# Kernel optimization log

Hardware: AMD Instinct MI355X
Metric: run time of the kernel (lower is better)

## Reference

```python
import jax, jax.numpy as jnp
import numpy as np


def setup_inputs() -> dict:
    key = jax.random.key(0)
    k1, k2, k3 = jax.random.split(key, 3)
    B, N, D = 4, 4096, 1024
    x = jax.random.normal(k1, (B, N, D), dtype=jnp.float32)
    # torch nn.Linear default init ~ U(-1/sqrt(D), 1/sqrt(D)); scale normals similarly
    scale = 1.0 / np.sqrt(D)
    Wq = jax.random.normal(k2, (D, D), dtype=jnp.float32) * scale
    Wk = jax.random.normal(k3, (D, D), dtype=jnp.float32) * scale
    return {"x": x, "Wq": Wq, "Wk": Wk}


def reference(x, Wq, Wk):
    # torch Linear: y = x @ W.T (weight shape [out, in])
    D = x.shape[-1]
    q = jnp.einsum('bnd,ed->bne', x, Wq)  # [B,N,D]
    k = jnp.einsum('bnd,ed->bne', x, Wk)  # [B,N,D]
    scores = jnp.einsum('bqd,bkd->bqk', q, k) / jnp.sqrt(jnp.float32(D))
    attn = jax.nn.softmax(scores, axis=-1)  # [B,N,N]
    return jnp.einsum('bqk,bkd->bqd', attn, x)
```

## Files before the change

### kernel.cpp

```cpp
#include <hip/hip_runtime.h>
#include <stdint.h>
#include <math.h>

typedef __attribute__((ext_vector_type(8))) short short8;
typedef __attribute__((ext_vector_type(4))) float fx4;
typedef unsigned int u32;

#define MFMA16(a, b, c) __builtin_amdgcn_mfma_f32_16x16x32_bf16(a, b, c, 0, 0, 0)
#define SCL 0.04508422002777948f

#define CFENCE asm volatile("" ::: "memory")

__device__ __forceinline__ unsigned short f2bfu(float f) {
  unsigned u = __builtin_bit_cast(unsigned, f);
  u += 0x7fffu + ((u >> 16) & 1u);
  return (unsigned short)(u >> 16);
}

__device__ __forceinline__ float fast_exp2(float x) {
  float r;
  asm("v_exp_f32 %0, %1" : "=v"(r) : "v"(x));
  return r;
}

__device__ __forceinline__ void gl_lds16(const void* g, void* l) {
  __builtin_amdgcn_global_load_lds(
      (const __attribute__((address_space(1))) u32*)g,
      (__attribute__((address_space(3))) u32*)l, 16, 0, 0);
}

__device__ __forceinline__ void barx() {
  CFENCE;
  __builtin_amdgcn_s_barrier();
  CFENCE;
}

__global__ __launch_bounds__(256) void prep_kernel(const float* __restrict__ x,
                                                   unsigned short* __restrict__ xT,
                                                   unsigned short* __restrict__ xbf) {
  __shared__ float tile[64 * 65];
  const int b = blockIdx.z, n0 = blockIdx.x * 64, d0 = blockIdx.y * 64;
  const int tid = threadIdx.x;
  const float* xb = x + ((size_t)b * 4096 + n0) * 1024 + d0;
#pragma unroll
  for (int i = 0; i < 4; i++) {
    int idx = tid + 256 * i;
    int r = idx >> 4, c4 = (idx & 15) * 4;
    const float4 v = *(const float4*)(xb + (size_t)r * 1024 + c4);
    float* tp = &tile[r * 65 + c4];
    tp[0] = v.x; tp[1] = v.y; tp[2] = v.z; tp[3] = v.w;
    uint2 pkt;
    pkt.x = (u32)f2bfu(v.x) | ((u32)f2bfu(v.y) << 16);
    pkt.y = (u32)f2bfu(v.z) | ((u32)f2bfu(v.w) << 16);
    *(uint2*)(xbf + ((size_t)b * 4096 + n0 + r) * 1024 + d0 + c4) = pkt;
  }
  __syncthreads();
  unsigned short* xo = xT + ((size_t)b * 1024 + d0) * 4096 + n0;
#pragma unroll
  for (int i = 0; i < 4; i++) {
    int idx = tid + 256 * i;
    int dr = idx >> 4, n4 = (idx & 15) * 4;
    unsigned short h0 = f2bfu(tile[(n4 + 0) * 65 + dr]);
    unsigned short h1 = f2bfu(tile[(n4 + 1) * 65 + dr]);
    unsigned short h2 = f2bfu(tile[(n4 + 2) * 65 + dr]);
    unsigned short h3 = f2bfu(tile[(n4 + 3) * 65 + dr]);
    uint2 pkt;
    pkt.x = (u32)h0 | ((u32)h1 << 16);
    pkt.y = (u32)h2 | ((u32)h3 << 16);
    *(uint2*)(xo + (size_t)dr * 4096 + n4) = pkt;
  }
}

__global__ __launch_bounds__(256) void wconv_kernel(const float* __restrict__ Wq,
                                                    const float* __restrict__ Wk,
                                                    unsigned short* __restrict__ Wqb,
                                                    unsigned short* __restrict__ Wkb) {
  int gid = blockIdx.x * 256 + threadIdx.x;
  const float* s = (gid < 262144) ? Wq : Wk;
  unsigned short* d = (gid < 262144) ? Wqb : Wkb;
  int off = (gid & 262143) * 4;
  const float4 v = *(const float4*)(s + off);
  uint2 pkt;
  pkt.x = (u32)f2bfu(v.x) | ((u32)f2bfu(v.y) << 16);
  pkt.y = (u32)f2bfu(v.z) | ((u32)f2bfu(v.w) << 16);
  *(uint2*)(d + off) = pkt;
}


template <int ONES, int NT, int LDA, int LDB>
__device__ __forceinline__ void core128(const unsigned short* __restrict__ Ab,
                                        const unsigned short* __restrict__ Bb,
                                        short* lds, fx4 (&acc)[4][4], fx4 (&accl)[4]) {
  constexpr int BUFB = 49152;
  const int tid = threadIdx.x;
  const int wave = tid >> 6, lane = tid & 63;
  const int wm = wave >> 1, wn = wave & 1;
  const int quad = lane >> 4, l16 = lane & 15;
  char* lp = (char*)lds;

  const int sr0 = tid >> 3, so0 = (tid & 7) ^ (sr0 & 7);
  const int ga0 = sr0 * LDA + so0 * 8;
  const int ga1 = ga0 + 64 * LDA;
  const int gb0 = sr0 * LDB + so0 * 8;
  const int ld0 = tid * 16;

  const int cst0 = (quad ^ (l16 & 7)) * 16;
  const int cst1 = ((4 + quad) ^ (l16 & 7)) * 16;
  const int arb = (wm >> 1) * 16384 + (wm & 1) * 8192 + l16 * 128;
  const int brb = 32768 + wn * 8192 + l16 * 128;

  short8 ones;
#pragma unroll
  for (int i = 0; i < 8; i++) ones[i] = (short)0x3F80;
#pragma unroll
  for (int i = 0; i < 4; i++) {
    accl[i] = (fx4)0.f;
#pragma unroll
    for (int j = 0; j < 4; j++) acc[i][j] = (fx4)0.f;
  }

#define PV_STGA(halfb, rowadd, bufb, kte)                                          \
  do {                                                                             \
    gl_lds16(Ab + (size_t)(rowadd) * LDA + (kte) + ga0, lp + (bufb) + (halfb) + ld0); \
    gl_lds16(Ab + (size_t)(rowadd) * LDA + (kte) + ga1,                            \
             lp + (bufb) + (halfb) + ld0 + 8192);                                  \
  } while (0)
#define PV_STGB(halfb, rowadd, bufb, kte) \
  gl_lds16(Bb + (size_t)(rowadd) * LDB + (kte) + gb0, lp + (bufb) + 32768 + (halfb) + ld0)

  PV_STGB(0, 0, 0, 0);
  PV_STGA(0, 0, 0, 0);
  PV_STGA(16384, 128, 0, 0);
  PV_STGB(8192, 64, 0, 0);
  PV_STGB(0, 0, BUFB, 64);
  PV_STGA(0, 0, BUFB, 64);
  asm volatile("s_waitcnt vmcnt(3)" ::: "memory");
  barx();

  short8 af[4], bf0[4], bf1[4];
  for (int t = 0; t < NT; ++t) {
    const int cbo = (t & 1) * BUFB, nbo = cbo ^ BUFB;
    const int kt1 = ((t + 1) & (NT - 1)) * 64;
    const int kt2 = ((t + 2) & (NT - 1)) * 64;
#pragma unroll
    for (int mt = 0; mt < 2; mt++) {
      af[2 * mt] = *(const short8*)(lp + cbo + arb + mt * 2048 + cst0);
      af[2 * mt + 1] = *(const short8*)(lp + cbo + arb + mt * 2048 + cst1);
    }
#pragma unroll
    for (int nt = 0; nt < 2; nt++) {
      bf0[2 * nt] = *(const short8*)(lp + cbo + brb + nt * 2048 + cst0);
      bf0[2 * nt + 1] = *(const short8*)(lp + cbo + brb + nt * 2048 + cst1);
    }
    PV_STGA(16384, 128, nbo, kt1);
    barx();
    __builtin_amdgcn_s_setprio(1);
#pragma unroll
    for (int mt = 0; mt < 2; mt++) {
#pragma unroll
      for (int nt = 0; nt < 2; nt++) {
        acc[mt][nt] = MFMA16(af[2 * mt], bf0[2 * nt], acc[mt][nt]);
        acc[mt][nt] = MFMA16(af[2 * mt + 1], bf0[2 * nt + 1], acc[mt][nt]);
      }
      if (ONES) {
        accl[mt] = MFMA16(af[2 * mt], ones, accl[mt]);
        accl[mt] = MFMA16(af[2 * mt + 1], ones, accl[mt]);
      }
    }
    __builtin_amdgcn_s_setprio(0);
    barx();
#pragma unroll
    for (int nt = 0; nt < 2; nt++) {
      bf1[2 * nt] = *(const short8*)(lp + cbo + brb + (nt + 2) * 2048 + cst0);
      bf1[2 * nt + 1] = *(const short8*)(lp + cbo + brb + (nt + 2) * 2048 + cst1);
    }
    PV_STGB(8192, 64, nbo, kt1);
    barx();
    __builtin_amdgcn_s_setprio(1);
#pragma unroll
    for (int mt = 0; mt < 2; mt++)
#pragma unroll
      for (int nt = 0; nt < 2; nt++) {
        acc[mt][nt + 2] = MFMA16(af[2 * mt], bf1[2 * nt], acc[mt][nt + 2]);
        acc[mt][nt + 2] = MFMA16(af[2 * mt + 1], bf1[2 * nt + 1], acc[mt][nt + 2]);
      }
    __builtin_amdgcn_s_setprio(0);
    barx();
#pragma unroll
    for (int mt = 0; mt < 2; mt++) {
      af[2 * mt] = *(const short8*)(lp + cbo + arb + (mt + 2) * 2048 + cst0);
      af[2 * mt + 1] = *(const short8*)(lp + cbo + arb + (mt + 2) * 2048 + cst1);
    }
    PV_STGB(0, 0, cbo, kt2);
    barx();
    __builtin_amdgcn_s_setprio(1);
#pragma unroll
    for (int mt = 0; mt < 2; mt++) {
#pragma unroll
      for (int nt = 0; nt < 2; nt++) {
        acc[mt + 2][nt + 2] = MFMA16(af[2 * mt], bf1[2 * nt], acc[mt + 2][nt + 2]);
        acc[mt + 2][nt + 2] = MFMA16(af[2 * mt + 1], bf1[2 * nt + 1], acc[mt + 2][nt + 2]);
      }
      if (ONES) {
        accl[mt + 2] = MFMA16(af[2 * mt], ones, accl[mt + 2]);
        accl[mt + 2] = MFMA16(af[2 * mt + 1], ones, accl[mt + 2]);
      }
    }
    __builtin_amdgcn_s_setprio(0);
    barx();
    PV_STGA(0, 0, cbo, kt2);
    asm volatile("s_waitcnt vmcnt(3)" ::: "memory");
    barx();
    __builtin_amdgcn_s_setprio(1);
#pragma unroll
    for (int mt = 0; mt < 2; mt++)
#pragma unroll
      for (int nt = 0; nt < 2; nt++) {
        acc[mt + 2][nt] = MFMA16(af[2 * mt], bf0[2 * nt], acc[mt + 2][nt]);
        acc[mt + 2][nt] = MFMA16(af[2 * mt + 1], bf0[2 * nt + 1], acc[mt + 2][nt]);
      }
    __builtin_amdgcn_s_setprio(0);
    barx();
  }
#undef PV_STGA
#undef PV_STGB
}

__global__ __launch_bounds__(512) void proj_kernel(
    const unsigned short* __restrict__ xbf, const unsigned short* __restrict__ Wqb,
    const unsigned short* __restrict__ Wkb, unsigned short* __restrict__ Qo,
    unsigned short* __restrict__ Ko) {
  __shared__ __attribute__((aligned(16))) short lds[49152];
  const unsigned short* Wb = blockIdx.z ? Wkb : Wqb;
  unsigned short* O = blockIdx.z ? Ko : Qo;
  const int m0 = blockIdx.x * 256, e0 = blockIdx.y * 128;
  fx4 acc[4][4], accl[4];
  core128<0, 16, 1024, 1024>(xbf + (size_t)m0 * 1024, Wb + (size_t)e0 * 1024, lds, acc, accl);
  const int wave = threadIdx.x >> 6, lane = threadIdx.x & 63;
  const int wm = wave >> 1, wn = wave & 1;
  const int quad = lane >> 4, l16 = lane & 15;
#pragma unroll
  for (int mt = 0; mt < 4; mt++) {
    const int row = m0 + wm * 64 + mt * 16 + quad * 4;
#pragma unroll
    for (int nt = 0; nt < 4; nt++) {
      const int col = e0 + wn * 64 + nt * 16 + l16;
      unsigned short* op = O + (size_t)row * 1024 + col;
#pragma unroll
      for (int i = 0; i < 4; i++) op[(size_t)i * 1024] = f2bfu(acc[mt][nt][i]);
    }
  }
}

__global__ __launch_bounds__(512) void pv_kernel(
    const unsigned short* __restrict__ P, const unsigned short* __restrict__ xT,
    unsigned short* __restrict__ Ost, int bbase) {
  __shared__ __attribute__((aligned(16))) short lds[49152];
  const int bz = blockIdx.z, b = bbase + bz;
  const int m0 = blockIdx.x * 256, e0 = blockIdx.y * 128;
  const unsigned short* Ab = P + (size_t)bz * 4096 * 4096 + (size_t)m0 * 4096;
  const unsigned short* Bb = xT + (size_t)b * 1024 * 4096 + (size_t)e0 * 4096;
  fx4 acc[4][4], accl[4];
  core128<1, 64, 4096, 4096>(Ab, Bb, lds, acc, accl);
  unsigned short* O = Ost + (size_t)b * 4096 * 1024;
  const int wave = threadIdx.x >> 6, lane = threadIdx.x & 63;
  const int wm = wave >> 1, wn = wave & 1;
  const int quad = lane >> 4, l16 = lane & 15;
#pragma unroll
  for (int mt = 0; mt < 4; mt++) {
    const int row = m0 + wm * 64 + mt * 16 + quad * 4;
    const fx4 li = accl[mt];
    fx4 r;
#pragma unroll
    for (int i = 0; i < 4; i++) r[i] = __builtin_amdgcn_rcpf(li[i]);
#pragma unroll
    for (int nt = 0; nt < 4; nt++) {
      const int col = e0 + wn * 64 + nt * 16 + l16;
      unsigned short* op = O + (size_t)row * 1024 + col;
#pragma unroll
      for (int i = 0; i < 4; i++) op[(size_t)i * 1024] = f2bfu(acc[mt][nt][i] * r[i]);
    }
  }
}

__global__ __launch_bounds__(512) void qk_kernel(
    const unsigned short* __restrict__ Qb, const unsigned short* __restrict__ Kb,
    unsigned short* __restrict__ Pp, int bbase) {
  constexpr int NT = 16;
  __shared__ __attribute__((aligned(16))) short lds[65536];
  const int bz = blockIdx.z, b = bbase + bz;
  const unsigned short* A = Qb + (size_t)b * 4096 * 1024;
  const unsigned short* Bm = Kb + (size_t)b * 4096 * 1024;
  unsigned short* Pb = Pp + (size_t)bz * 4096 * 4096;
  const int m0 = blockIdx.x * 256, n0 = blockIdx.y * 256;
  const int tid = threadIdx.x;
  const int wave = tid >> 6, lane = tid & 63;
  const int wm = wave >> 2, wn = wave & 3;
  const int quad = lane >> 4, l16 = lane & 15;
  char* lp = (char*)lds;

  const unsigned short* Ab = A + (size_t)m0 * 1024;
  const unsigned short* Bb = Bm + (size_t)n0 * 1024;
  const int sr0 = tid >> 3, so0 = (tid & 7) ^ (sr0 & 7);
  const int ga0 = sr0 * 1024 + so0 * 8;
  const int ga1 = ga0 + 64 * 1024;
  const int ld0 = tid * 16;

  const int cst0 = (quad ^ (l16 & 7)) * 16;
  const int cst1 = ((4 + quad) ^ (l16 & 7)) * 16;
  const int arb = wm * 16384 + l16 * 128;
  const int brb = 32768 + (wn >> 1) * 16384 + (wn & 1) * 8192 + l16 * 128;

  fx4 acc[8][4];
#pragma unroll
  for (int i = 0; i < 8; i++)
#pragma unroll
    for (int j = 0; j < 4; j++) acc[i][j] = (fx4)0.f;

#define QK_STG(OPb, halfb, rowadd, bufb, kte)                                       \
  do {                                                                              \
    gl_lds16(OPb + (size_t)(rowadd) * 1024 + (kte) + ga0, lp + (bufb) + (halfb) + ld0); \
    gl_lds16(OPb + (size_t)(rowadd) * 1024 + (kte) + ga1,                           \
             lp + (bufb) + (halfb) + ld0 + 8192);                                   \
  } while (0)

  QK_STG(Bb, 32768, 0, 0, 0);
  QK_STG(Ab, 0, 0, 0, 0);
  QK_STG(Ab, 16384, 128, 0, 0);
  QK_STG(Bb, 49152, 128, 0, 0);
  QK_STG(Bb, 32768, 0, 65536, 64);
  QK_STG(Ab, 0, 0, 65536, 64);
  asm volatile("s_waitcnt vmcnt(4)" ::: "memory");
  barx();

  short8 af[8], bf0[4], bf1[4];
  for (int t = 0; t < NT; ++t) {
    const int cbo = (t & 1) * 65536, nbo = cbo ^ 65536;
    const int kt1 = ((t + 1) & (NT - 1)) * 64;
    const int kt2 = ((t + 2) & (NT - 1)) * 64;
#pragma unroll
    for (int mt = 0; mt < 4; mt++) {
      af[2 * mt] = *(const short8*)(lp + cbo + arb + mt * 2048 + cst0);
      af[2 * mt + 1] = *(const short8*)(lp + cbo + arb + mt * 2048 + cst1);
    }
#pragma unroll
    for (int nt = 0; nt < 2; nt++) {
      bf0[2 * nt] = *(const short8*)(lp + cbo + brb + nt * 2048 + cst0);
      bf0[2 * nt + 1] = *(const short8*)(lp + cbo + brb + nt * 2048 + cst1);
    }
    QK_STG(Ab, 16384, 128, nbo, kt1);
    barx();
    __builtin_amdgcn_s_setprio(1);
#pragma unroll
    for (int mt = 0; mt < 4; mt++)
#pragma unroll
      for (int nt = 0; nt < 2; nt++) {
        acc[mt][nt] = MFMA16(af[2 * mt], bf0[2 * nt], acc[mt][nt]);
        acc[mt][nt] = MFMA16(af[2 * mt + 1], bf0[2 * nt + 1], acc[mt][nt]);
      }
    __builtin_amdgcn_s_setprio(0);
    barx();
#pragma unroll
    for (int nt = 0; nt < 2; nt++) {
      bf1[2 * nt] = *(const short8*)(lp + cbo + brb + (nt + 2) * 2048 + cst0);
      bf1[2 * nt + 1] = *(const short8*)(lp + cbo + brb + (nt + 2) * 2048 + cst1);
    }
    QK_STG(Bb, 49152, 128, nbo, kt1);
    barx();
    __builtin_amdgcn_s_setprio(1);
#pragma unroll
    for (int mt = 0; mt < 4; mt++)
#pragma unroll
      for (int nt = 0; nt < 2; nt++) {
        acc[mt][nt + 2] = MFMA16(af[2 * mt], bf1[2 * nt], acc[mt][nt + 2]);
        acc[mt][nt + 2] = MFMA16(af[2 * mt + 1], bf1[2 * nt + 1], acc[mt][nt + 2]);
      }
    __builtin_amdgcn_s_setprio(0);
    barx();
#pragma unroll
    for (int mt = 0; mt < 4; mt++) {
      af[2 * mt] = *(const short8*)(lp + cbo + arb + (mt + 4) * 2048 + cst0);
      af[2 * mt + 1] = *(const short8*)(lp + cbo + arb + (mt + 4) * 2048 + cst1);
    }
    QK_STG(Bb, 32768, 0, cbo, kt2);
    barx();
    __builtin_amdgcn_s_setprio(1);
#pragma unroll
    for (int mt = 0; mt < 4; mt++)
#pragma unroll
      for (int nt = 0; nt < 2; nt++) {
        acc[mt + 4][nt + 2] = MFMA16(af[2 * mt], bf1[2 * nt], acc[mt + 4][nt + 2]);
        acc[mt + 4][nt + 2] = MFMA16(af[2 * mt + 1], bf1[2 * nt + 1], acc[mt + 4][nt + 2]);
      }
    __builtin_amdgcn_s_setprio(0);
    barx();
    QK_STG(Ab, 0, 0, cbo, kt2);
    asm volatile("s_waitcnt vmcnt(4)" ::: "memory");
    barx();
    __builtin_amdgcn_s_setprio(1);
#pragma unroll
    for (int mt = 0; mt < 4; mt++)
#pragma unroll
      for (int nt = 0; nt < 2; nt++) {
        acc[mt + 4][nt] = MFMA16(af[2 * mt], bf0[2 * nt], acc[mt + 4][nt]);
        acc[mt + 4][nt] = MFMA16(af[2 * mt + 1], bf0[2 * nt + 1], acc[mt + 4][nt]);
      }
    __builtin_amdgcn_s_setprio(0);
    barx();
  }
#undef QK_STG
#pragma unroll
  for (int mt = 0; mt < 8; mt++) {
    const int row = m0 + wm * 128 + mt * 16 + quad * 4;
#pragma unroll
    for (int nt = 0; nt < 4; nt++) {
      const int col = n0 + wn * 64 + nt * 16 + l16;
      unsigned short* pp = Pb + (size_t)row * 4096 + col;
#pragma unroll
      for (int i = 0; i < 4; i++)
        pp[(size_t)i * 4096] = f2bfu(fast_exp2(acc[mt][nt][i] * SCL));
    }
  }
}

__global__ __launch_bounds__(256) void fin_kernel(const uint4* __restrict__ Ost,
                                                  float4* __restrict__ out) {
  size_t t = (size_t)blockIdx.x * 256 + threadIdx.x;
  const uint4 v = Ost[t];
  float4 o0, o1;
  o0.x = __builtin_bit_cast(float, v.x << 16);
  o0.y = __builtin_bit_cast(float, v.x & 0xffff0000u);
  o0.z = __builtin_bit_cast(float, v.y << 16);
  o0.w = __builtin_bit_cast(float, v.y & 0xffff0000u);
  o1.x = __builtin_bit_cast(float, v.z << 16);
  o1.y = __builtin_bit_cast(float, v.z & 0xffff0000u);
  o1.z = __builtin_bit_cast(float, v.w << 16);
  o1.w = __builtin_bit_cast(float, v.w & 0xffff0000u);
  out[t * 2] = o0;
  out[t * 2 + 1] = o1;
}

extern "C" void kernel_launch(void* const* d_in, const int* in_sizes, int n_in,
                              void* d_out, int out_size, void* d_ws, size_t ws_size,
                              hipStream_t stream) {
  const float* x = (const float*)d_in[0];
  const float* Wq = (const float*)d_in[1];
  const float* Wk = (const float*)d_in[2];
  char* ws = (char*)d_ws;
  unsigned short* xT = (unsigned short*)ws;
  unsigned short* Qb = (unsigned short*)(ws + (size_t)33554432);
  unsigned short* Kb = (unsigned short*)(ws + (size_t)67108864);
  unsigned short* Ost = Qb;
  unsigned short* xbf = (unsigned short*)d_out;
  unsigned short* Wqb = (unsigned short*)((char*)d_out + (size_t)33554432);
  unsigned short* Wkb = (unsigned short*)((char*)d_out + (size_t)35651584);
  unsigned short* Pp = (unsigned short*)d_out;

  hipLaunchKernelGGL(prep_kernel, dim3(64, 16, 4), dim3(256), 0, stream, x, xT, xbf);
  hipLaunchKernelGGL(wconv_kernel, dim3(2048), dim3(256), 0, stream, Wq, Wk, Wqb, Wkb);
  hipLaunchKernelGGL(proj_kernel, dim3(64, 8, 2), dim3(512), 0, stream, xbf, Wqb, Wkb, Qb, Kb);
  hipLaunchKernelGGL(qk_kernel, dim3(16, 16, 2), dim3(512), 0, stream, Qb, Kb, Pp, 0);
  hipLaunchKernelGGL(pv_kernel, dim3(16, 8, 2), dim3(512), 0, stream, Pp, xT, Ost, 0);
  hipLaunchKernelGGL(qk_kernel, dim3(16, 16, 2), dim3(512), 0, stream, Qb, Kb, Pp, 2);
  hipLaunchKernelGGL(pv_kernel, dim3(16, 8, 2), dim3(512), 0, stream, Pp, xT, Ost, 2);
  hipLaunchKernelGGL(fin_kernel, dim3(8192), dim3(256), 0, stream,
                     (const uint4*)Ost, (float4*)d_out);
}
```

Baseline: 497.1 us.

## Share 256x256 GEMM core for proj and QK; restage PV pipeline

The QK kernel's 256x256 tile mainloop is pulled into a shared core256 routine, and the projection kernel now uses it with 256-wide output tiles instead of 128, halving the grid in that dimension. This increases operand reuse per block at the cost of more LDS and registers per block. The PV kernel gets its own inlined mainloop with two MFMA phases per k-step instead of four. It also reorders its async loads and waitcnt thresholds, meant to reduce barrier count and improve overlap.

```diff
diff --git a/kernel.cpp b/kernel.cpp
--- a/kernel.cpp
+++ b/kernel.cpp
@@ -86,12 +86,186 @@
   *(uint2*)(d + off) = pkt;
 }
 
-
-template <int ONES, int NT, int LDA, int LDB>
-__device__ __forceinline__ void core128(const unsigned short* __restrict__ Ab,
+__device__ __forceinline__ void core256(const unsigned short* __restrict__ Ab,
                                         const unsigned short* __restrict__ Bb,
-                                        short* lds, fx4 (&acc)[4][4], fx4 (&accl)[4]) {
-  constexpr int BUFB = 49152;
+                                        char* lp, fx4 (&acc)[8][4]) {
+  constexpr int NT = 16;
+  const int tid = threadIdx.x;
+  const int wave = tid >> 6, lane = tid & 63;
+  const int wm = wave >> 2, wn = wave & 3;
+  const int quad = lane >> 4, l16 = lane & 15;
+
+  const int sr0 = tid >> 3, so0 = (tid & 7) ^ (sr0 & 7);
+  const int ga0 = sr0 * 1024 + so0 * 8;
+  const int ga1 = ga0 + 64 * 1024;
+  const int ld0 = tid * 16;
+
+  const int cst0 = (quad ^ (l16 & 7)) * 16;
+  const int cst1 = ((4 + quad) ^ (l16 & 7)) * 16;
+  const int arb = wm * 16384 + l16 * 128;
+  const int brb = 32768 + (wn >> 1) * 16384 + (wn & 1) * 8192 + l16 * 128;
+
+#pragma unroll
+  for (int i = 0; i < 8; i++)
+#pragma unroll
+    for (int j = 0; j < 4; j++) acc[i][j] = (fx4)0.f;
+
+#define C_STG(OPb, halfb, rowadd, bufb, kte)                                        \
+  do {                                                                              \
+    gl_lds16(OPb + (size_t)(rowadd) * 1024 + (kte) + ga0, lp + (bufb) + (halfb) + ld0); \
+    gl_lds16(OPb + (size_t)(rowadd) * 1024 + (kte) + ga1,                           \
+             lp + (bufb) + (halfb) + ld0 + 8192);                                   \
+  } while (0)
+
+  C_STG(Bb, 32768, 0, 0, 0);
+  C_STG(Ab, 0, 0, 0, 0);
+  C_STG(Ab, 16384, 128, 0, 0);
+  C_STG(Bb, 49152, 128, 0, 0);
+  C_STG(Bb, 32768, 0, 65536, 64);
+  C_STG(Ab, 0, 0, 65536, 64);
+  asm volatile("s_waitcnt vmcnt(4)" ::: "memory");
+  barx();
+
+  short8 af[8], bf0[4], bf1[4];
+  for (int t = 0; t < NT; ++t) {
+    const int cbo = (t & 1) * 65536, nbo = cbo ^ 65536;
+    const int kt1 = ((t + 1) & (NT - 1)) * 64;
+    const int kt2 = ((t + 2) & (NT - 1)) * 64;
+#pragma unroll
+    for (int mt = 0; mt < 4; mt++) {
+      af[2 * mt] = *(const short8*)(lp + cbo + arb + mt * 2048 + cst0);
+      af[2 * mt + 1] = *(const short8*)(lp + cbo + arb + mt * 2048 + cst1);
+    }
+#pragma unroll
+    for (int nt = 0; nt < 2; nt++) {
+      bf0[2 * nt] = *(const short8*)(lp + cbo + brb + nt * 2048 + cst0);
+      bf0[2 * nt + 1] = *(const short8*)(lp + cbo + brb + nt * 2048 + cst1);
+    }
+    C_STG(Ab, 16384, 128, nbo, kt1);
+    barx();
+    __builtin_amdgcn_s_setprio(1);
+#pragma unroll
+    for (int mt = 0; mt < 4; mt++)
+#pragma unroll
+      for (int nt = 0; nt < 2; nt++) {
+        acc[mt][nt] = MFMA16(af[2 * mt], bf0[2 * nt], acc[mt][nt]);
+        acc[mt][nt] = MFMA16(af[2 * mt + 1], bf0[2 * nt + 1], acc[mt][nt]);
+      }
+    __builtin_amdgcn_s_setprio(0);
+    barx();
+#pragma unroll
+    for (int nt = 0; nt < 2; nt++) {
+      bf1[2 * nt] = *(const short8*)(lp + cbo + brb + (nt + 2) * 2048 + cst0);
+      bf1[2 * nt + 1] = *(const short8*)(lp + cbo + brb + (nt + 2) * 2048 + cst1);
+    }
+    C_STG(Bb, 49152, 128, nbo, kt1);
+    barx();
+    __builtin_amdgcn_s_setprio(1);
+#pragma unroll
+    for (int mt = 0; mt < 4; mt++)
+#pragma unroll
+      for (int nt = 0; nt < 2; nt++) {
+        acc[mt][nt + 2] = MFMA16(af[2 * mt], bf1[2 * nt], acc[mt][nt + 2]);
+        acc[mt][nt + 2] = MFMA16(af[2 * mt + 1], bf1[2 * nt + 1], acc[mt][nt + 2]);
+      }
+    __builtin_amdgcn_s_setprio(0);
+    barx();
+#pragma unroll
+    for (int mt = 0; mt < 4; mt++) {
+      af[2 * mt] = *(const short8*)(lp + cbo + arb + (mt + 4) * 2048 + cst0);
+      af[2 * mt + 1] = *(const short8*)(lp + cbo + arb + (mt + 4) * 2048 + cst1);
+    }
+    C_STG(Bb, 32768, 0, cbo, kt2);
+    barx();
+    __builtin_amdgcn_s_setprio(1);
+#pragma unroll
+    for (int mt = 0; mt < 4; mt++)
+#pragma unroll
+      for (int nt = 0; nt < 2; nt++) {
+        acc[mt + 4][nt + 2] = MFMA16(af[2 * mt], bf1[2 * nt], acc[mt + 4][nt + 2]);
+        acc[mt + 4][nt + 2] = MFMA16(af[2 * mt + 1], bf1[2 * nt + 1], acc[mt + 4][nt + 2]);
+      }
+    __builtin_amdgcn_s_setprio(0);
+    barx();
+    C_STG(Ab, 0, 0, cbo, kt2);
+    asm volatile("s_waitcnt vmcnt(4)" ::: "memory");
+    barx();
+    __builtin_amdgcn_s_setprio(1);
+#pragma unroll
+    for (int mt = 0; mt < 4; mt++)
+#pragma unroll
+      for (int nt = 0; nt < 2; nt++) {
+        acc[mt + 4][nt] = MFMA16(af[2 * mt], bf0[2 * nt], acc[mt + 4][nt]);
+        acc[mt + 4][nt] = MFMA16(af[2 * mt + 1], bf0[2 * nt + 1], acc[mt + 4][nt]);
+      }
+    __builtin_amdgcn_s_setprio(0);
+    barx();
+  }
+#undef C_STG
+}
+
+__global__ __launch_bounds__(512) void proj_kernel(
+    const unsigned short* __restrict__ xbf, const unsigned short* __restrict__ Wqb,
+    const unsigned short* __restrict__ Wkb, unsigned short* __restrict__ Qo,
+    unsigned short* __restrict__ Ko) {
+  __shared__ __attribute__((aligned(16))) short lds[65536];
+  const unsigned short* Wb = blockIdx.z ? Wkb : Wqb;
+  unsigned short* O = blockIdx.z ? Ko : Qo;
+  const int m0 = blockIdx.x * 256, e0 = blockIdx.y * 256;
+  fx4 acc[8][4];
+  core256(xbf + (size_t)m0 * 1024, Wb + (size_t)e0 * 1024, (char*)lds, acc);
+  const int wave = threadIdx.x >> 6, lane = threadIdx.x & 63;
+  const int wm = wave >> 2, wn = wave & 3;
+  const int quad = lane >> 4, l16 = lane & 15;
+#pragma unroll
+  for (int mt = 0; mt < 8; mt++) {
+    const int row = m0 + wm * 128 + mt * 16 + quad * 4;
+#pragma unroll
+    for (int nt = 0; nt < 4; nt++) {
+      const int col = e0 + wn * 64 + nt * 16 + l16;
+      unsigned short* op = O + (size_t)row * 1024 + col;
+#pragma unroll
+      for (int i = 0; i < 4; i++) op[(size_t)i * 1024] = f2bfu(acc[mt][nt][i]);
+    }
+  }
+}
+
+__global__ __launch_bounds__(512) void qk_kernel(
+    const unsigned short* __restrict__ Qb, const unsigned short* __restrict__ Kb,
+    unsigned short* __restrict__ Pp, int bbase) {
+  __shared__ __attribute__((aligned(16))) short lds[65536];
+  const int bz = blockIdx.z, b = bbase + bz;
+  unsigned short* Pb = Pp + (size_t)bz * 4096 * 4096;
+  const int m0 = blockIdx.x * 256, n0 = blockIdx.y * 256;
+  fx4 acc[8][4];
+  core256(Qb + (size_t)b * 4096 * 1024 + (size_t)m0 * 1024,
+          Kb + (size_t)b * 4096 * 1024 + (size_t)n0 * 1024, (char*)lds, acc);
+  const int wave = threadIdx.x >> 6, lane = threadIdx.x & 63;
+  const int wm = wave >> 2, wn = wave & 3;
+  const int quad = lane >> 4, l16 = lane & 15;
+#pragma unroll
+  for (int mt = 0; mt < 8; mt++) {
+    const int row = m0 + wm * 128 + mt * 16 + quad * 4;
+#pragma unroll
+    for (int nt = 0; nt < 4; nt++) {
+      const int col = n0 + wn * 64 + nt * 16 + l16;
+      unsigned short* pp = Pb + (size_t)row * 4096 + col;
+#pragma unroll
+      for (int i = 0; i < 4; i++)
+        pp[(size_t)i * 4096] = f2bfu(fast_exp2(acc[mt][nt][i] * SCL));
+    }
+  }
+}
+
+__global__ __launch_bounds__(512) void pv_kernel(
+    const unsigned short* __restrict__ P, const unsigned short* __restrict__ xT,
+    unsigned short* __restrict__ Ost, int bbase) {
+  constexpr int NT = 64, BUFB = 49152;
+  __shared__ __attribute__((aligned(16))) short lds[49152];
+  const int bz = blockIdx.z, b = bbase + bz;
+  const int m0 = blockIdx.x * 256, e0 = blockIdx.y * 128;
+  const unsigned short* Ab = P + (size_t)bz * 4096 * 4096 + (size_t)m0 * 4096;
+  const unsigned short* Bb = xT + (size_t)b * 1024 * 4096 + (size_t)e0 * 4096;
   const int tid = threadIdx.x;
   const int wave = tid >> 6, lane = tid & 63;
   const int wm = wave >> 1, wn = wave & 1;
@@ -99,9 +273,8 @@
   char* lp = (char*)lds;
 
   const int sr0 = tid >> 3, so0 = (tid & 7) ^ (sr0 & 7);
-  const int ga0 = sr0 * LDA + so0 * 8;
-  const int ga1 = ga0 + 64 * LDA;
-  const int gb0 = sr0 * LDB + so0 * 8;
+  const int g0 = sr0 * 4096 + so0 * 8;
+  const int g1 = g0 + 64 * 4096;
   const int ld0 = tid * 16;
 
   const int cst0 = (quad ^ (l16 & 7)) * 16;
@@ -112,6 +285,8 @@
   short8 ones;
 #pragma unroll
   for (int i = 0; i < 8; i++) ones[i] = (short)0x3F80;
+
+  fx4 acc[4][4], accl[4];
 #pragma unroll
   for (int i = 0; i < 4; i++) {
     accl[i] = (fx4)0.f;
@@ -119,153 +294,82 @@
     for (int j = 0; j < 4; j++) acc[i][j] = (fx4)0.f;
   }
 
-#define PV_STGA(halfb, rowadd, bufb, kte)                                          \
-  do {                                                                             \
-    gl_lds16(Ab + (size_t)(rowadd) * LDA + (kte) + ga0, lp + (bufb) + (halfb) + ld0); \
-    gl_lds16(Ab + (size_t)(rowadd) * LDA + (kte) + ga1,                            \
-             lp + (bufb) + (halfb) + ld0 + 8192);                                  \
+#define PV_STGA(bufb, kte)                                                   \
+  do {                                                                       \
+    gl_lds16(Ab + (size_t)(kte) + g0, lp + (bufb) + ld0);                    \
+    gl_lds16(Ab + (size_t)(kte) + g1, lp + (bufb) + ld0 + 8192);             \
+    gl_lds16(Ab + (size_t)128 * 4096 + (kte) + g0, lp + (bufb) + 16384 + ld0); \
+    gl_lds16(Ab + (size_t)128 * 4096 + (kte) + g1,                           \
+             lp + (bufb) + 16384 + ld0 + 8192);                              \
   } while (0)
-#define PV_STGB(halfb, rowadd, bufb, kte) \
-  gl_lds16(Bb + (size_t)(rowadd) * LDB + (kte) + gb0, lp + (bufb) + 32768 + (halfb) + ld0)
-
-  PV_STGB(0, 0, 0, 0);
-  PV_STGA(0, 0, 0, 0);
-  PV_STGA(16384, 128, 0, 0);
-  PV_STGB(8192, 64, 0, 0);
-  PV_STGB(0, 0, BUFB, 64);
-  PV_STGA(0, 0, BUFB, 64);
-  asm volatile("s_waitcnt vmcnt(3)" ::: "memory");
+#define PV_STGB0(bufb, kte) gl_lds16(Bb + (size_t)(kte) + g0, lp + (bufb) + 32768 + ld0)
+#define PV_STGB1(bufb, kte) \
+  gl_lds16(Bb + (size_t)64 * 4096 + (kte) + g0, lp + (bufb) + 40960 + ld0)
+
+  PV_STGA(0, 0);
+  PV_STGB0(0, 0);
+  PV_STGB1(0, 0);
+  PV_STGA(BUFB, 64);
+  PV_STGB0(BUFB, 64);
+  asm volatile("s_waitcnt vmcnt(5)" ::: "memory");
   barx();
 
-  short8 af[4], bf0[4], bf1[4];
+  short8 af[8], bfv[4];
   for (int t = 0; t < NT; ++t) {
     const int cbo = (t & 1) * BUFB, nbo = cbo ^ BUFB;
     const int kt1 = ((t + 1) & (NT - 1)) * 64;
     const int kt2 = ((t + 2) & (NT - 1)) * 64;
 #pragma unroll
-    for (int mt = 0; mt < 2; mt++) {
+    for (int mt = 0; mt < 4; mt++) {
       af[2 * mt] = *(const short8*)(lp + cbo + arb + mt * 2048 + cst0);
       af[2 * mt + 1] = *(const short8*)(lp + cbo + arb + mt * 2048 + cst1);
     }
 #pragma unroll
     for (int nt = 0; nt < 2; nt++) {
-      bf0[2 * nt] = *(const short8*)(lp + cbo + brb + nt * 2048 + cst0);
-      bf0[2 * nt + 1] = *(const short8*)(lp + cbo + brb + nt * 2048 + cst1);
-    }
-    PV_STGA(16384, 128, nbo, kt1);
-    barx();
-    __builtin_amdgcn_s_setprio(1);
-#pragma unroll
-    for (int mt = 0; mt < 2; mt++) {
-#pragma unroll
-      for (int nt = 0; nt < 2; nt++) {
-        acc[mt][nt] = MFMA16(af[2 * mt], bf0[2 * nt], acc[mt][nt]);
-        acc[mt][nt] = MFMA16(af[2 * mt + 1], bf0[2 * nt + 1], acc[mt][nt]);
-      }
-      if (ONES) {
-        accl[mt] = MFMA16(af[2 * mt], ones, accl[mt]);
-        accl[mt] = MFMA16(af[2 * mt + 1], ones, accl[mt]);
-      }
+      bfv[2 * nt] = *(const short8*)(lp + cbo + brb + nt * 2048 + cst0);
+      bfv[2 * nt + 1] = *(const short8*)(lp + cbo + brb + nt * 2048 + cst1);
+    }
+    PV_STGB1(nbo, kt1);
+    asm volatile("s_waitcnt vmcnt(5)" ::: "memory");
+    barx();
+    __builtin_amdgcn_s_setprio(1);
+#pragma unroll
+    for (int mt = 0; mt < 4; mt++) {
+#pragma unroll
+      for (int nt = 0; nt < 2; nt++) {
+        acc[mt][nt] = MFMA16(af[2 * mt], bfv[2 * nt], acc[mt][nt]);
+        acc[mt][nt] = MFMA16(af[2 * mt + 1], bfv[2 * nt + 1], acc[mt][nt]);
+      }
+      accl[mt] = MFMA16(af[2 * mt], ones, accl[mt]);
+      accl[mt] = MFMA16(af[2 * mt + 1], ones, accl[mt]);
     }
     __builtin_amdgcn_s_setprio(0);
     barx();
 #pragma unroll
     for (int nt = 0; nt < 2; nt++) {
-      bf1[2 * nt] = *(const short8*)(lp + cbo + brb + (nt + 2) * 2048 + cst0);
-      bf1[2 * nt + 1] = *(const short8*)(lp + cbo + brb + (nt + 2) * 2048 + cst1);
-    }
-    PV_STGB(8192, 64, nbo, kt1);
-    barx();
-    __builtin_amdgcn_s_setprio(1);
-#pragma unroll
-    for (int mt = 0; mt < 2; mt++)
-#pragma unroll
-      for (int nt = 0; nt < 2; nt++) {
-        acc[mt][nt + 2] = MFMA16(af[2 * mt], bf1[2 * nt], acc[mt][nt + 2]);
-        acc[mt][nt + 2] = MFMA16(af[2 * mt + 1], bf1[2 * nt + 1], acc[mt][nt + 2]);
-      }
-    __builtin_amdgcn_s_setprio(0);
-    barx();
-#pragma unroll
-    for (int mt = 0; mt < 2; mt++) {
-      af[2 * mt] = *(const short8*)(lp + cbo + arb + (mt + 2) * 2048 + cst0);
-      af[2 * mt + 1] = *(const short8*)(lp + cbo + arb + (mt + 2) * 2048 + cst1);
-    }
-    PV_STGB(0, 0, cbo, kt2);
-    barx();
-    __builtin_amdgcn_s_setprio(1);
-#pragma unroll
-    for (int mt = 0; mt < 2; mt++) {
-#pragma unroll
-      for (int nt = 0; nt < 2; nt++) {
-        acc[mt + 2][nt + 2] = MFMA16(af[2 * mt], bf1[2 * nt], acc[mt + 2][nt + 2]);
-        acc[mt + 2][nt + 2] = MFMA16(af[2 * mt + 1], bf1[2 * nt + 1], acc[mt + 2][nt + 2]);
-      }
-      if (ONES) {
-        accl[mt + 2] = MFMA16(af[2 * mt], ones, accl[mt + 2]);
-        accl[mt + 2] = MFMA16(af[2 * mt + 1], ones, accl[mt + 2]);
-      }
-    }
-    __builtin_amdgcn_s_setprio(0);
-    barx();
-    PV_STGA(0, 0, cbo, kt2);
-    asm volatile("s_waitcnt vmcnt(3)" ::: "memory");
-    barx();
-    __builtin_amdgcn_s_setprio(1);
-#pragma unroll
-    for (int mt = 0; mt < 2; mt++)
-#pragma unroll
-      for (int nt = 0; nt < 2; nt++) {
-        acc[mt + 2][nt] = MFMA16(af[2 * mt], bf0[2 * nt], acc[mt + 2][nt]);
-        acc[mt + 2][nt] = MFMA16(af[2 * mt + 1], bf0[2 * nt + 1], acc[mt + 2][nt]);
+      bfv[2 * nt] = *(const short8*)(lp + cbo + brb + (nt + 2) * 2048 + cst0);
+      bfv[2 * nt + 1] = *(const short8*)(lp + cbo + brb + (nt + 2) * 2048 + cst1);
+    }
+    PV_STGA(cbo, kt2);
+    PV_STGB0(cbo, kt2);
+    asm volatile("s_waitcnt vmcnt(6)" ::: "memory");
+    barx();
+    __builtin_amdgcn_s_setprio(1);
+#pragma unroll
+    for (int mt = 0; mt < 4; mt++)
+#pragma unroll
+      for (int nt = 0; nt < 2; nt++) {
+        acc[mt][nt + 2] = MFMA16(af[2 * mt], bfv[2 * nt], acc[mt][nt + 2]);
+        acc[mt][nt + 2] = MFMA16(af[2 * mt + 1], bfv[2 * nt + 1], acc[mt][nt + 2]);
       }
     __builtin_amdgcn_s_setprio(0);
     barx();
   }
 #undef PV_STGA
-#undef PV_STGB
-}
-
-__global__ __launch_bounds__(512) void proj_kernel(
-    const unsigned short* __restrict__ xbf, const unsigned short* __restrict__ Wqb,
-    const unsigned short* __restrict__ Wkb, unsigned short* __restrict__ Qo,
-    unsigned short* __restrict__ Ko) {
-  __shared__ __attribute__((aligned(16))) short lds[49152];
-  const unsigned short* Wb = blockIdx.z ? Wkb : Wqb;
-  unsigned short* O = blockIdx.z ? Ko : Qo;
-  const int m0 = blockIdx.x * 256, e0 = blockIdx.y * 128;
-  fx4 acc[4][4], accl[4];
-  core128<0, 16, 1024, 1024>(xbf + (size_t)m0 * 1024, Wb + (size_t)e0 * 1024, lds, acc, accl);
-  const int wave = threadIdx.x >> 6, lane = threadIdx.x & 63;
-  const int wm = wave >> 1, wn = wave & 1;
-  const int quad = lane >> 4, l16 = lane & 15;
-#pragma unroll
-  for (int mt = 0; mt < 4; mt++) {
-    const int row = m0 + wm * 64 + mt * 16 + quad * 4;
-#pragma unroll
-    for (int nt = 0; nt < 4; nt++) {
-      const int col = e0 + wn * 64 + nt * 16 + l16;
-      unsigned short* op = O + (size_t)row * 1024 + col;
-#pragma unroll
-      for (int i = 0; i < 4; i++) op[(size_t)i * 1024] = f2bfu(acc[mt][nt][i]);
-    }
-  }
-}
-
-__global__ __launch_bounds__(512) void pv_kernel(
-    const unsigned short* __restrict__ P, const unsigned short* __restrict__ xT,
-    unsigned short* __restrict__ Ost, int bbase) {
-  __shared__ __attribute__((aligned(16))) short lds[49152];
-  const int bz = blockIdx.z, b = bbase + bz;
-  const int m0 = blockIdx.x * 256, e0 = blockIdx.y * 128;
-  const unsigned short* Ab = P + (size_t)bz * 4096 * 4096 + (size_t)m0 * 4096;
-  const unsigned short* Bb = xT + (size_t)b * 1024 * 4096 + (size_t)e0 * 4096;
-  fx4 acc[4][4], accl[4];
-  core128<1, 64, 4096, 4096>(Ab, Bb, lds, acc, accl);
+#undef PV_STGB0
+#undef PV_STGB1
+
   unsigned short* O = Ost + (size_t)b * 4096 * 1024;
-  const int wave = threadIdx.x >> 6, lane = threadIdx.x & 63;
-  const int wm = wave >> 1, wn = wave & 1;
-  const int quad = lane >> 4, l16 = lane & 15;
 #pragma unroll
   for (int mt = 0; mt < 4; mt++) {
     const int row = m0 + wm * 64 + mt * 16 + quad * 4;
@@ -279,146 +383,6 @@
       unsigned short* op = O + (size_t)row * 1024 + col;
 #pragma unroll
       for (int i = 0; i < 4; i++) op[(size_t)i * 1024] = f2bfu(acc[mt][nt][i] * r[i]);
-    }
-  }
-}
-
-__global__ __launch_bounds__(512) void qk_kernel(
-    const unsigned short* __restrict__ Qb, const unsigned short* __restrict__ Kb,
-    unsigned short* __restrict__ Pp, int bbase) {
-  constexpr int NT = 16;
-  __shared__ __attribute__((aligned(16))) short lds[65536];
-  const int bz = blockIdx.z, b = bbase + bz;
-  const unsigned short* A = Qb + (size_t)b * 4096 * 1024;
-  const unsigned short* Bm = Kb + (size_t)b * 4096 * 1024;
-  unsigned short* Pb = Pp + (size_t)bz * 4096 * 4096;
-  const int m0 = blockIdx.x * 256, n0 = blockIdx.y * 256;
-  const int tid = threadIdx.x;
-  const int wave = tid >> 6, lane = tid & 63;
-  const int wm = wave >> 2, wn = wave & 3;
-  const int quad = lane >> 4, l16 = lane & 15;
-  char* lp = (char*)lds;
-
-  const unsigned short* Ab = A + (size_t)m0 * 1024;
-  const unsigned short* Bb = Bm + (size_t)n0 * 1024;
-  const int sr0 = tid >> 3, so0 = (tid & 7) ^ (sr0 & 7);
-  const int ga0 = sr0 * 1024 + so0 * 8;
-  const int ga1 = ga0 + 64 * 1024;
-  const int ld0 = tid * 16;
-
-  const int cst0 = (quad ^ (l16 & 7)) * 16;
-  const int cst1 = ((4 + quad) ^ (l16 & 7)) * 16;
-  const int arb = wm * 16384 + l16 * 128;
-  const int brb = 32768 + (wn >> 1) * 16384 + (wn & 1) * 8192 + l16 * 128;
-
-  fx4 acc[8][4];
-#pragma unroll
-  for (int i = 0; i < 8; i++)
-#pragma unroll
-    for (int j = 0; j < 4; j++) acc[i][j] = (fx4)0.f;
-
-#define QK_STG(OPb, halfb, rowadd, bufb, kte)                                       \
-  do {                                                                              \
-    gl_lds16(OPb + (size_t)(rowadd) * 1024 + (kte) + ga0, lp + (bufb) + (halfb) + ld0); \
-    gl_lds16(OPb + (size_t)(rowadd) * 1024 + (kte) + ga1,                           \
-             lp + (bufb) + (halfb) + ld0 + 8192);                                   \
-  } while (0)
-
-  QK_STG(Bb, 32768, 0, 0, 0);
-  QK_STG(Ab, 0, 0, 0, 0);
-  QK_STG(Ab, 16384, 128, 0, 0);
-  QK_STG(Bb, 49152, 128, 0, 0);
-  QK_STG(Bb, 32768, 0, 65536, 64);
-  QK_STG(Ab, 0, 0, 65536, 64);
-  asm volatile("s_waitcnt vmcnt(4)" ::: "memory");
-  barx();
-
-  short8 af[8], bf0[4], bf1[4];
-  for (int t = 0; t < NT; ++t) {
-    const int cbo = (t & 1) * 65536, nbo = cbo ^ 65536;
-    const int kt1 = ((t + 1) & (NT - 1)) * 64;
-    const int kt2 = ((t + 2) & (NT - 1)) * 64;
-#pragma unroll
-    for (int mt = 0; mt < 4; mt++) {
-      af[2 * mt] = *(const short8*)(lp + cbo + arb + mt * 2048 + cst0);
-      af[2 * mt + 1] = *(const short8*)(lp + cbo + arb + mt * 2048 + cst1);
-    }
-#pragma unroll
-    for (int nt = 0; nt < 2; nt++) {
-      bf0[2 * nt] = *(const short8*)(lp + cbo + brb + nt * 2048 + cst0);
-      bf0[2 * nt + 1] = *(const short8*)(lp + cbo + brb + nt * 2048 + cst1);
-    }
-    QK_STG(Ab, 16384, 128, nbo, kt1);
-    barx();
-    __builtin_amdgcn_s_setprio(1);
-#pragma unroll
-    for (int mt = 0; mt < 4; mt++)
-#pragma unroll
-      for (int nt = 0; nt < 2; nt++) {
-        acc[mt][nt] = MFMA16(af[2 * mt], bf0[2 * nt], acc[mt][nt]);
-        acc[mt][nt] = MFMA16(af[2 * mt + 1], bf0[2 * nt + 1], acc[mt][nt]);
-      }
-    __builtin_amdgcn_s_setprio(0);
-    barx();
-#pragma unroll
-    for (int nt = 0; nt < 2; nt++) {
-      bf1[2 * nt] = *(const short8*)(lp + cbo + brb + (nt + 2) * 2048 + cst0);
-      bf1[2 * nt + 1] = *(const short8*)(lp + cbo + brb + (nt + 2) * 2048 + cst1);
-    }
-    QK_STG(Bb, 49152, 128, nbo, kt1);
-    barx();
-    __builtin_amdgcn_s_setprio(1);
-#pragma unroll
-    for (int mt = 0; mt < 4; mt++)
-#pragma unroll
-      for (int nt = 0; nt < 2; nt++) {
-        acc[mt][nt + 2] = MFMA16(af[2 * mt], bf1[2 * nt], acc[mt][nt + 2]);
-        acc[mt][nt + 2] = MFMA16(af[2 * mt + 1], bf1[2 * nt + 1], acc[mt][nt + 2]);
-      }
-    __builtin_amdgcn_s_setprio(0);
-    barx();
-#pragma unroll
-    for (int mt = 0; mt < 4; mt++) {
-      af[2 * mt] = *(const short8*)(lp + cbo + arb + (mt + 4) * 2048 + cst0);
-      af[2 * mt + 1] = *(const short8*)(lp + cbo + arb + (mt + 4) * 2048 + cst1);
-    }
-    QK_STG(Bb, 32768, 0, cbo, kt2);
-    barx();
-    __builtin_amdgcn_s_setprio(1);
-#pragma unroll
-    for (int mt = 0; mt < 4; mt++)
-#pragma unroll
-      for (int nt = 0; nt < 2; nt++) {
-        acc[mt + 4][nt + 2] = MFMA16(af[2 * mt], bf1[2 * nt], acc[mt + 4][nt + 2]);
-        acc[mt + 4][nt + 2] = MFMA16(af[2 * mt + 1], bf1[2 * nt + 1], acc[mt + 4][nt + 2]);
-      }
-    __builtin_amdgcn_s_setprio(0);
-    barx();
-    QK_STG(Ab, 0, 0, cbo, kt2);
-    asm volatile("s_waitcnt vmcnt(4)" ::: "memory");
-    barx();
-    __builtin_amdgcn_s_setprio(1);
-#pragma unroll
-    for (int mt = 0; mt < 4; mt++)
-#pragma unroll
-      for (int nt = 0; nt < 2; nt++) {
-        acc[mt + 4][nt] = MFMA16(af[2 * mt], bf0[2 * nt], acc[mt + 4][nt]);
-        acc[mt + 4][nt] = MFMA16(af[2 * mt + 1], bf0[2 * nt + 1], acc[mt + 4][nt]);
-      }
-    __builtin_amdgcn_s_setprio(0);
-    barx();
-  }
-#undef QK_STG
-#pragma unroll
-  for (int mt = 0; mt < 8; mt++) {
-    const int row = m0 + wm * 128 + mt * 16 + quad * 4;
-#pragma unroll
-    for (int nt = 0; nt < 4; nt++) {
-      const int col = n0 + wn * 64 + nt * 16 + l16;
-      unsigned short* pp = Pb + (size_t)row * 4096 + col;
-#pragma unroll
-      for (int i = 0; i < 4; i++)
-        pp[(size_t)i * 4096] = f2bfu(fast_exp2(acc[mt][nt][i] * SCL));
     }
   }
 }
@@ -458,7 +422,7 @@
 
   hipLaunchKernelGGL(prep_kernel, dim3(64, 16, 4), dim3(256), 0, stream, x, xT, xbf);
   hipLaunchKernelGGL(wconv_kernel, dim3(2048), dim3(256), 0, stream, Wq, Wk, Wqb, Wkb);
-  hipLaunchKernelGGL(proj_kernel, dim3(64, 8, 2), dim3(512), 0, stream, xbf, Wqb, Wkb, Qb, Kb);
+  hipLaunchKernelGGL(proj_kernel, dim3(64, 4, 2), dim3(512), 0, stream, xbf, Wqb, Wkb, Qb, Kb);
   hipLaunchKernelGGL(qk_kernel, dim3(16, 16, 2), dim3(512), 0, stream, Qb, Kb, Pp, 0);
   hipLaunchKernelGGL(pv_kernel, dim3(16, 8, 2), dim3(512), 0, stream, Pp, xT, Ost, 0);
   hipLaunchKernelGGL(qk_kernel, dim3(16, 16, 2), dim3(512), 0, stream, Qb, Kb, Pp, 2);
```

New measurement: 474.5 us. -4.5%, faster.
